# Kernel optimization log

Hardware: AMD Instinct MI355X
Metric: run time of the kernel (lower is better)

Reference implementation:

```python
import jax, jax.numpy as jnp
import numpy as np

COS_EPS = 1e-8   # torch F.cosine_similarity norm clamp
SIM_EPS = 1e-6   # +1e-6 added to every cosine similarity in get_cossim
LOG_EPS = 1e-6   # +1e-6 inside log in calc_loss


def setup_inputs() -> dict:
    key = jax.random.key(0)
    k1, = jax.random.split(key, 1)
    N, M, D = 1024, 16, 512
    embeddings = jax.random.normal(k1, (N, M, D), dtype=jnp.float32)
    w = jnp.asarray(10.0, dtype=jnp.float32)
    b = jnp.asarray(-5.0, dtype=jnp.float32)
    return {"embeddings": embeddings, "w": w, "b": b}


def _unit(x):
    n = jnp.sqrt(jnp.sum(x * x, axis=-1, keepdims=True))
    return x / jnp.maximum(n, COS_EPS)


def _ge2e_loss(embeddings, w, b):
    N, M, D = embeddings.shape
    e_unit = _unit(embeddings)                              # [N, M, D]

    # full centroids (mean over utterances)
    centroids = jnp.mean(embeddings, axis=1)                # [N, D]
    c_unit = _unit(centroids)                               # [N, D]

    # cosine sim of every utterance vs every speaker centroid
    cossim = jnp.einsum('nmd,kd->nmk', e_unit, c_unit)      # [N, M, N]

    # leave-one-out centroid for own-speaker entries (self-exclusion)
    loo = (jnp.sum(embeddings, axis=1, keepdims=True) - embeddings) / (M - 1)  # [N, M, D]
    diag = jnp.sum(e_unit * _unit(loo), axis=-1)            # [N, M]

    idx = jnp.arange(N)
    cossim = cossim.at[idx, :, idx].set(diag)
    cossim = cossim + SIM_EPS

    sim_matrix = w * cossim + b                             # [N, M, N]

    pos = sim_matrix[idx, :, idx]                           # [N, M]
    neg = jnp.log(jnp.sum(jnp.exp(sim_matrix), axis=2) + LOG_EPS)  # [N, M]
    return jnp.sum(neg - pos)


def reference(embeddings, w, b):
    return _ge2e_loss(embeddings, w, b)
```

## Files before the change

kernel.cpp:

```cpp
#include <hip/hip_runtime.h>

#define N_SPK 1024
#define M_UTT 16
#define D_DIM 512

typedef __attribute__((ext_vector_type(8))) short bf16x8;
typedef __attribute__((ext_vector_type(4))) float f32x4;

__device__ __forceinline__ float wave_sum64(float v) {
  #pragma unroll
  for (int off = 32; off >= 1; off >>= 1) v += __shfl_xor(v, off, 64);
  return v;
}

__device__ __forceinline__ unsigned short f2bf(float x) {
  unsigned int u = __float_as_uint(x);
  unsigned int r = (u + 0x7FFFu + ((u >> 16) & 1u)) >> 16;
  return (unsigned short)r;
}

__device__ __forceinline__ unsigned int pack_bf16(float a, float b) {
  return (unsigned int)f2bf(a) | ((unsigned int)f2bf(b) << 16);
}

__device__ __forceinline__ void gload_lds16(const void* g, void* l) {
  __builtin_amdgcn_global_load_lds(
      (const __attribute__((address_space(1))) void*)g,
      (__attribute__((address_space(3))) void*)l, 16, 0, 0);
}

__device__ __forceinline__ void lgkm0() {
  asm volatile("s_waitcnt lgkmcnt(0)" ::: "memory");
}

__global__ __launch_bounds__(256) void prep_kernel(
    const float* __restrict__ emb, const float* __restrict__ wp,
    const float* __restrict__ bp, unsigned int* __restrict__ eU,
    unsigned int* __restrict__ cU, float* __restrict__ pos_out)
{
  const int n = blockIdx.x;
  const int t = threadIdx.x;
  __shared__ float es[M_UTT * D_DIM];
  __shared__ float Sd[D_DIM];
  __shared__ float red[4];
  __shared__ float inv_s[M_UTT];

  const float* base = emb + (size_t)n * (M_UTT * D_DIM);
  #pragma unroll
  for (int i = 0; i < 8; ++i) {
    int s = t + i * 256;
    reinterpret_cast<float4*>(es)[s] = reinterpret_cast<const float4*>(base)[s];
  }
  __syncthreads();

  #pragma unroll
  for (int rep = 0; rep < 2; ++rep) {
    int d = t + rep * 256;
    float s = 0.f;
    #pragma unroll
    for (int m = 0; m < M_UTT; ++m) s += es[m * D_DIM + d];
    Sd[d] = s;
  }
  __syncthreads();

  float p = 0.f;
  #pragma unroll
  for (int rep = 0; rep < 2; ++rep) {
    int d = t + rep * 256;
    float c = Sd[d] * (1.f / M_UTT);
    p += c * c;
  }
  p = wave_sum64(p);
  if ((t & 63) == 0) red[t >> 6] = p;
  __syncthreads();
  float cn2 = red[0] + red[1] + red[2] + red[3];
  float invc = 1.f / fmaxf(sqrtf(cn2), 1e-8f);

  {
    int d = t * 2;
    float c0 = Sd[d] * (1.f / M_UTT) * invc;
    float c1 = Sd[d + 1] * (1.f / M_UTT) * invc;
    cU[n * 256 + t] = pack_bf16(c0, c1);
  }

  const int wid = t >> 6, lane = t & 63;
  const float w = *wp, b = *bp;
  for (int m = wid; m < M_UTT; m += 4) {
    float dot = 0.f, ne = 0.f, nl = 0.f;
    #pragma unroll
    for (int r = 0; r < 8; ++r) {
      int d = lane + r * 64;
      float e = es[m * D_DIM + d];
      float l = Sd[d] - e;
      dot += e * l; ne += e * e; nl += l * l;
    }
    dot = wave_sum64(dot); ne = wave_sum64(ne); nl = wave_sum64(nl);
    if (lane == 0) {
      float inv_e = 1.f / fmaxf(sqrtf(ne), 1e-8f);
      float inv_l = 1.f / fmaxf(sqrtf(nl) * (1.f / (M_UTT - 1)), 1e-8f);
      float diag = dot * (1.f / (M_UTT - 1)) * inv_e * inv_l;
      pos_out[n * M_UTT + m] = w * (diag + 1e-6f) + b;
      inv_s[m] = inv_e;
    }
  }
  __syncthreads();

  #pragma unroll
  for (int i = 0; i < 16; ++i) {
    int p2 = t + i * 256;
    int m = p2 >> 8;
    int d = (p2 & 255) * 2;
    float sc = inv_s[m];
    float x0 = es[m * D_DIM + d] * sc;
    float x1 = es[m * D_DIM + d + 1] * sc;
    eU[(size_t)n * 4096 + p2] = pack_bf16(x0, x1);
  }
}

#define NKT 8

struct Pipe {
  const char* gA;
  const char* gB;
  char* lA;
  char* lB;
};

__device__ __forceinline__ void stage_A(const Pipe& p, int tt, int hi) {
  char* d = p.lA + ((tt & 1) << 15) + hi * 16384;
  const char* g = p.gA + tt * 128 + hi * 131072;
  gload_lds16(g, d);
  gload_lds16(g + 65536, d + 8192);
}
__device__ __forceinline__ void stage_B(const Pipe& p, int tt, int hi) {
  char* d = p.lB + ((tt & 1) << 15) + hi * 16384;
  const char* g = p.gB + tt * 128 + hi * 131072;
  gload_lds16(g, d);
  gload_lds16(g + 65536, d + 8192);
}

template <int MI0, int NJ0>
__device__ __forceinline__ void mfma_quad(f32x4 acc[8][4], const bf16x8 af[4][2],
                                          const bf16x8 bf[4][2]) {
  __builtin_amdgcn_s_setprio(1);
  #pragma unroll
  for (int kk = 0; kk < 2; ++kk)
    #pragma unroll
    for (int mi = 0; mi < 4; ++mi)
      #pragma unroll
      for (int nj = 0; nj < 2; ++nj)
        acc[MI0 + mi][NJ0 + nj] = __builtin_amdgcn_mfma_f32_16x16x32_bf16(
            af[mi][kk], bf[NJ0 + nj][kk], acc[MI0 + mi][NJ0 + nj], 0, 0, 0);
  __builtin_amdgcn_s_setprio(0);
}

__global__ __launch_bounds__(512, 2) void mfma_kernel(
    const char* __restrict__ eU, const char* __restrict__ cU,
    const float* __restrict__ pos, const float* __restrict__ wp,
    const float* __restrict__ bp, float* __restrict__ partial)
{
  __shared__ char ldsA[65536];
  __shared__ char ldsB[65536];
  __shared__ float pos_l[256];
  __shared__ float rowsum[4][256];

  const int t = threadIdx.x;
  const int lane = t & 63;
  const int wv = t >> 6;
  const int wm = wv >> 2, wn = wv & 3;

  const int bid = blockIdx.x;
  const int sw = (bid & 7) * 32 + (bid >> 3);
  const int cb = sw & 3, rb = sw >> 2;
  const int row0 = rb * 256, col0 = cb * 256;

  const float w = *wp, b = *bp;
  const float bb = w * 1e-6f + b;

  if (t < 256) pos_l[t] = pos[row0 + t];

  Pipe p;
  {
    const int rowl = wv * 8 + (lane >> 3);
    const int seg = (lane & 7) ^ (lane >> 3);
    p.gA = eU + (size_t)(row0 + rowl) * 1024 + seg * 16;
    p.gB = cU + (size_t)(col0 + rowl) * 1024 + seg * 16;
    p.lA = ldsA + wv * 1024;
    p.lB = ldsB + wv * 1024;
  }

  const int j16 = lane & 15, g = lane >> 4;
  const int afb0 = (wm * 128 + j16) * 128 + (((0 * 4 + g) ^ (lane & 7)) * 16);
  const int afb1 = (wm * 128 + j16) * 128 + (((1 * 4 + g) ^ (lane & 7)) * 16);
  const int bfb0 = (wn * 64 + j16) * 128 + (((0 * 4 + g) ^ (lane & 7)) * 16);
  const int bfb1 = (wn * 64 + j16) * 128 + (((1 * 4 + g) ^ (lane & 7)) * 16);

  f32x4 acc[8][4] = {};
  bf16x8 af[4][2], bf[4][2];

  __syncthreads();

  stage_B(p, 0, 0); stage_B(p, 0, 1);
  stage_A(p, 0, 0); stage_A(p, 0, 1);
  stage_B(p, 1, 0); stage_B(p, 1, 1);
  asm volatile("s_waitcnt vmcnt(4)" ::: "memory");
  __builtin_amdgcn_s_barrier();

  for (int j = 0; j < NKT; ++j) {
    const int bo = (j & 1) << 15;
    #pragma unroll
    for (int a = 0; a < 4; ++a) {
      af[a][0] = *reinterpret_cast<const bf16x8*>(ldsA + bo + afb0 + a * 2048);
      af[a][1] = *reinterpret_cast<const bf16x8*>(ldsA + bo + afb1 + a * 2048);
    }
    #pragma unroll
    for (int nq = 0; nq < 2; ++nq) {
      bf[nq][0] = *reinterpret_cast<const bf16x8*>(ldsB + bo + bfb0 + nq * 2048);
      bf[nq][1] = *reinterpret_cast<const bf16x8*>(ldsB + bo + bfb1 + nq * 2048);
    }
    if (j <= 6) stage_A(p, j + 1, 0);
    __builtin_amdgcn_s_barrier();
    lgkm0();
    mfma_quad<0, 0>(acc, af, bf);
    __builtin_amdgcn_s_barrier();
    #pragma unroll
    for (int nq = 2; nq < 4; ++nq) {
      bf[nq][0] = *reinterpret_cast<const bf16x8*>(ldsB + bo + bfb0 + nq * 2048);
      bf[nq][1] = *reinterpret_cast<const bf16x8*>(ldsB + bo + bfb1 + nq * 2048);
    }
    if (j <= 6) stage_A(p, j + 1, 1);
    __builtin_amdgcn_s_barrier();
    lgkm0();
    mfma_quad<0, 2>(acc, af, bf);
    __builtin_amdgcn_s_barrier();
    #pragma unroll
    for (int a = 0; a < 4; ++a) {
      af[a][0] = *reinterpret_cast<const bf16x8*>(ldsA + bo + afb0 + (a + 4) * 2048);
      af[a][1] = *reinterpret_cast<const bf16x8*>(ldsA + bo + afb1 + (a + 4) * 2048);
    }
    if (j <= 5) stage_B(p, j + 2, 0);
    __builtin_amdgcn_s_barrier();
    lgkm0();
    mfma_quad<4, 0>(acc, af, bf);
    __builtin_amdgcn_s_barrier();
    if (j <= 5) stage_B(p, j + 2, 1);
    if (j < 7) {
      if (j == 6) { asm volatile("s_waitcnt vmcnt(0)" ::: "memory"); }
      else        { asm volatile("s_waitcnt vmcnt(4)" ::: "memory"); }
    }
    __builtin_amdgcn_s_barrier();
    mfma_quad<4, 2>(acc, af, bf);
    __builtin_amdgcn_s_barrier();
  }

  float esum[8][4];
  #pragma unroll
  for (int mi = 0; mi < 8; ++mi)
    #pragma unroll
    for (int rg = 0; rg < 4; ++rg) esum[mi][rg] = 0.f;

  #pragma unroll
  for (int nj = 0; nj < 4; ++nj) {
    const int kg = col0 + wn * 64 + nj * 16 + (lane & 15);
    #pragma unroll
    for (int mi = 0; mi < 8; ++mi) {
      #pragma unroll
      for (int rg = 0; rg < 4; ++rg) {
        const int r_loc = wm * 128 + mi * 16 + (lane >> 4) * 4 + rg;
        float arg = w * acc[mi][nj][rg] + bb;
        if (kg == ((row0 + r_loc) >> 4)) arg = pos_l[r_loc];
        esum[mi][rg] += __expf(arg);
      }
    }
  }
  #pragma unroll
  for (int mi = 0; mi < 8; ++mi)
    #pragma unroll
    for (int rg = 0; rg < 4; ++rg) {
      float v = esum[mi][rg];
      v += __shfl_xor(v, 1, 64);
      v += __shfl_xor(v, 2, 64);
      v += __shfl_xor(v, 4, 64);
      v += __shfl_xor(v, 8, 64);
      esum[mi][rg] = v;
    }
  if ((lane & 15) == 0) {
    #pragma unroll
    for (int mi = 0; mi < 8; ++mi)
      #pragma unroll
      for (int rg = 0; rg < 4; ++rg)
        rowsum[wn][wm * 128 + mi * 16 + (lane >> 4) * 4 + rg] = esum[mi][rg];
  }
  __syncthreads();
  if (t < 256)
    partial[(size_t)cb * (N_SPK * M_UTT) + row0 + t] =
        rowsum[0][t] + rowsum[1][t] + rowsum[2][t] + rowsum[3][t];
}

__global__ __launch_bounds__(1024) void finalize_kernel(
    const float* __restrict__ partial, const float* __restrict__ pos,
    float* __restrict__ out)
{
  const int t = threadIdx.x;
  float v = 0.f;
  #pragma unroll
  for (int i = 0; i < 16; ++i) {
    const int r = t + i * 1024;
    float s = partial[r] + partial[16384 + r] + partial[32768 + r] +
              partial[49152 + r];
    v += logf(s + 1e-6f) - pos[r];
  }
  v = wave_sum64(v);
  __shared__ float red[16];
  if ((t & 63) == 0) red[t >> 6] = v;
  __syncthreads();
  if (t == 0) {
    float s = 0.f;
    #pragma unroll
    for (int i = 0; i < 16; ++i) s += red[i];
    out[0] = s;
  }
}

extern "C" void kernel_launch(void* const* d_in, const int* in_sizes, int n_in,
                              void* d_out, int out_size, void* d_ws, size_t ws_size,
                              hipStream_t stream) {
  const float* emb = (const float*)d_in[0];
  const float* wp  = (const float*)d_in[1];
  const float* bp  = (const float*)d_in[2];
  float* out = (float*)d_out;

  char* wsb = (char*)d_ws;
  unsigned int* eU  = (unsigned int*)wsb;
  unsigned int* cU  = (unsigned int*)(wsb + 16777216);
  float* pos        = (float*)(wsb + 16777216 + 1048576);
  float* partial    = (float*)(wsb + 16777216 + 1048576 + 65536);

  prep_kernel<<<N_SPK, 256, 0, stream>>>(emb, wp, bp, eU, cU, pos);
  mfma_kernel<<<256, 512, 0, stream>>>(
      (const char*)eU, (const char*)cU, pos, wp, bp, partial);
  finalize_kernel<<<1, 1024, 0, stream>>>(partial, pos, out);
}
```

Measured before the change: 44.93 us.

## Replace fine-grained interleaved staging with simple whole-tile double buffering

The GEMM main loop stops splitting each k-tile into four MFMA quadrants, each with its own barriers and partial global-to-LDS stages for A and B. It now issues one full A+B tile prefetch per iteration, and does a single vmcnt(0) wait and barrier at the top of the loop before two larger MFMA halves. The pos_l load moves after the loop, behind a __syncthreads. The aim is to cut barrier and waitcnt overhead, at the cost of coarser overlap: each iteration waits for its whole tile to land before computing.

Result: no change. 45.24 us (+0.7%).

```diff
diff --git a/kernel.cpp b/kernel.cpp
--- a/kernel.cpp
+++ b/kernel.cpp
@@ -27,10 +27,6 @@
   __builtin_amdgcn_global_load_lds(
       (const __attribute__((address_space(1))) void*)g,
       (__attribute__((address_space(3))) void*)l, 16, 0, 0);
-}
-
-__device__ __forceinline__ void lgkm0() {
-  asm volatile("s_waitcnt lgkmcnt(0)" ::: "memory");
 }
 
 __global__ __launch_bounds__(256) void prep_kernel(
@@ -126,21 +122,22 @@
   char* lB;
 };
 
-__device__ __forceinline__ void stage_A(const Pipe& p, int tt, int hi) {
-  char* d = p.lA + ((tt & 1) << 15) + hi * 16384;
-  const char* g = p.gA + tt * 128 + hi * 131072;
-  gload_lds16(g, d);
-  gload_lds16(g + 65536, d + 8192);
-}
-__device__ __forceinline__ void stage_B(const Pipe& p, int tt, int hi) {
-  char* d = p.lB + ((tt & 1) << 15) + hi * 16384;
-  const char* g = p.gB + tt * 128 + hi * 131072;
-  gload_lds16(g, d);
-  gload_lds16(g + 65536, d + 8192);
-}
-
-template <int MI0, int NJ0>
-__device__ __forceinline__ void mfma_quad(f32x4 acc[8][4], const bf16x8 af[4][2],
+__device__ __forceinline__ void stage_tile(const Pipe& p, int tt) {
+  const int bo = (tt & 1) << 15;
+  const char* gA = p.gA + tt * 128;
+  const char* gB = p.gB + tt * 128;
+  gload_lds16(gA,           p.lA + bo);
+  gload_lds16(gA + 65536,   p.lA + bo + 8192);
+  gload_lds16(gA + 131072,  p.lA + bo + 16384);
+  gload_lds16(gA + 196608,  p.lA + bo + 24576);
+  gload_lds16(gB,           p.lB + bo);
+  gload_lds16(gB + 65536,   p.lB + bo + 8192);
+  gload_lds16(gB + 131072,  p.lB + bo + 16384);
+  gload_lds16(gB + 196608,  p.lB + bo + 24576);
+}
+
+template <int MI0>
+__device__ __forceinline__ void mfma_half(f32x4 acc[8][4], const bf16x8 af[4][2],
                                           const bf16x8 bf[4][2]) {
   __builtin_amdgcn_s_setprio(1);
   #pragma unroll
@@ -148,9 +145,9 @@
     #pragma unroll
     for (int mi = 0; mi < 4; ++mi)
       #pragma unroll
-      for (int nj = 0; nj < 2; ++nj)
-        acc[MI0 + mi][NJ0 + nj] = __builtin_amdgcn_mfma_f32_16x16x32_bf16(
-            af[mi][kk], bf[NJ0 + nj][kk], acc[MI0 + mi][NJ0 + nj], 0, 0, 0);
+      for (int nj = 0; nj < 4; ++nj)
+        acc[MI0 + mi][nj] = __builtin_amdgcn_mfma_f32_16x16x32_bf16(
+            af[mi][kk], bf[nj][kk], acc[MI0 + mi][nj], 0, 0, 0);
   __builtin_amdgcn_s_setprio(0);
 }
 
@@ -177,8 +174,6 @@
   const float w = *wp, b = *bp;
   const float bb = w * 1e-6f + b;
 
-  if (t < 256) pos_l[t] = pos[row0 + t];
-
   Pipe p;
   {
     const int rowl = wv * 8 + (lane >> 3);
@@ -198,60 +193,35 @@
   f32x4 acc[8][4] = {};
   bf16x8 af[4][2], bf[4][2];
 
-  __syncthreads();
-
-  stage_B(p, 0, 0); stage_B(p, 0, 1);
-  stage_A(p, 0, 0); stage_A(p, 0, 1);
-  stage_B(p, 1, 0); stage_B(p, 1, 1);
-  asm volatile("s_waitcnt vmcnt(4)" ::: "memory");
-  __builtin_amdgcn_s_barrier();
+  stage_tile(p, 0);
 
   for (int j = 0; j < NKT; ++j) {
+    asm volatile("s_waitcnt vmcnt(0)" ::: "memory");
+    __builtin_amdgcn_s_barrier();
+    if (j < NKT - 1) stage_tile(p, j + 1);
+
     const int bo = (j & 1) << 15;
+    #pragma unroll
+    for (int nq = 0; nq < 4; ++nq) {
+      bf[nq][0] = *reinterpret_cast<const bf16x8*>(ldsB + bo + bfb0 + nq * 2048);
+      bf[nq][1] = *reinterpret_cast<const bf16x8*>(ldsB + bo + bfb1 + nq * 2048);
+    }
     #pragma unroll
     for (int a = 0; a < 4; ++a) {
       af[a][0] = *reinterpret_cast<const bf16x8*>(ldsA + bo + afb0 + a * 2048);
       af[a][1] = *reinterpret_cast<const bf16x8*>(ldsA + bo + afb1 + a * 2048);
     }
-    #pragma unroll
-    for (int nq = 0; nq < 2; ++nq) {
-      bf[nq][0] = *reinterpret_cast<const bf16x8*>(ldsB + bo + bfb0 + nq * 2048);
-      bf[nq][1] = *reinterpret_cast<const bf16x8*>(ldsB + bo + bfb1 + nq * 2048);
-    }
-    if (j <= 6) stage_A(p, j + 1, 0);
-    __builtin_amdgcn_s_barrier();
-    lgkm0();
-    mfma_quad<0, 0>(acc, af, bf);
-    __builtin_amdgcn_s_barrier();
-    #pragma unroll
-    for (int nq = 2; nq < 4; ++nq) {
-      bf[nq][0] = *reinterpret_cast<const bf16x8*>(ldsB + bo + bfb0 + nq * 2048);
-      bf[nq][1] = *reinterpret_cast<const bf16x8*>(ldsB + bo + bfb1 + nq * 2048);
-    }
-    if (j <= 6) stage_A(p, j + 1, 1);
-    __builtin_amdgcn_s_barrier();
-    lgkm0();
-    mfma_quad<0, 2>(acc, af, bf);
-    __builtin_amdgcn_s_barrier();
+    mfma_half<0>(acc, af, bf);
     #pragma unroll
     for (int a = 0; a < 4; ++a) {
       af[a][0] = *reinterpret_cast<const bf16x8*>(ldsA + bo + afb0 + (a + 4) * 2048);
       af[a][1] = *reinterpret_cast<const bf16x8*>(ldsA + bo + afb1 + (a + 4) * 2048);
     }
-    if (j <= 5) stage_B(p, j + 2, 0);
-    __builtin_amdgcn_s_barrier();
-    lgkm0();
-    mfma_quad<4, 0>(acc, af, bf);
-    __builtin_amdgcn_s_barrier();
-    if (j <= 5) stage_B(p, j + 2, 1);
-    if (j < 7) {
-      if (j == 6) { asm volatile("s_waitcnt vmcnt(0)" ::: "memory"); }
-      else        { asm volatile("s_waitcnt vmcnt(4)" ::: "memory"); }
-    }
-    __builtin_amdgcn_s_barrier();
-    mfma_quad<4, 2>(acc, af, bf);
-    __builtin_amdgcn_s_barrier();
-  }
+    mfma_half<4>(acc, af, bf);
+  }
+
+  if (t < 256) pos_l[t] = pos[row0 + t];
+  __syncthreads();
 
   float esum[8][4];
   #pragma unroll
```
